# Performance work log

Hardware: AMD Instinct MI355X
Metric: run time of the kernel (lower is better)

Reference implementation:

```python
import jax, jax.numpy as jnp
import numpy as np

TEMPERATURE = 0.07
N, D = 16384, 128
NUM_CLASSES = 100


def setup_inputs() -> dict:
    key = jax.random.key(0)
    kf, kl = jax.random.split(key)
    features = jax.random.normal(kf, (N, D), dtype=jnp.float32)
    labels = jax.random.randint(kl, (N,), 0, NUM_CLASSES, dtype=jnp.int64)
    return {"features": features, "labels": labels}


def reference(features, labels):
    # L2-normalize along feature dim (torch F.normalize, eps=1e-12)
    norm = jnp.linalg.norm(features, axis=1, keepdims=True)
    feats = features / jnp.maximum(norm, 1e-12)
    # [N, N] cosine similarity scaled by temperature
    sim = jnp.matmul(feats, feats.T) / TEMPERATURE
    # positive mask: same label, diagonal zeroed
    lab = labels.reshape(-1, 1)
    mask = (lab == lab.T).astype(sim.dtype)
    n = sim.shape[0]
    mask = mask * (1.0 - jnp.eye(n, dtype=sim.dtype))
    exp_sim = jnp.exp(sim)
    # denominator uses (1 - mask): all non-positive pairs INCLUDING the diagonal
    denom = jnp.sum(exp_sim * (1.0 - mask), axis=1)
    numer = jnp.sum(exp_sim * mask, axis=1)
    loss = -jnp.log(numer / denom + 1e-08)
    return jnp.mean(loss)
```

## Files before the change

### kernel.cpp

```cpp
#include <hip/hip_runtime.h>
#include <hip/hip_bf16.h>
#include <cstdint>
#include <cstddef>


#define N_ROWS 16384
#define DIM    128
#define TILE   128
#define NTILES (N_ROWS / TILE)

#define FEAT_SCALE 4.5398164f

typedef __attribute__((ext_vector_type(8))) short bf16x8;
typedef __attribute__((ext_vector_type(4))) float f32x4;

typedef const __attribute__((address_space(1))) unsigned int* gas_ptr;
typedef __attribute__((address_space(3))) unsigned int* las_ptr;

__global__ __launch_bounds__(256) void k_normalize(const float* __restrict__ F,
                                                   __hip_bfloat16* __restrict__ G) {
    int tid  = threadIdx.x;
    int lane = tid & 63;
    int wave = tid >> 6;
    int row  = blockIdx.x * 4 + wave;
    const float2* src = (const float2*)(F + (size_t)row * DIM) + lane;
    float2 x = *src;
    float s = x.x * x.x + x.y * x.y;
#pragma unroll
    for (int i = 1; i < 64; i <<= 1) s += __shfl_xor(s, i, 64);
    float scale = FEAT_SCALE / fmaxf(sqrtf(s), 1e-12f);
    __hip_bfloat162 h;
    h.x = __float2bfloat16(x.x * scale);
    h.y = __float2bfloat16(x.y * scale);
    ((__hip_bfloat162*)(G + (size_t)row * DIM))[lane] = h;
}

template<bool ATOM>
__global__ __launch_bounds__(256, 2) void k_tiles(const __hip_bfloat16* __restrict__ G,
                                                  const int* __restrict__ lab,
                                                  float* __restrict__ pNum,
                                                  float* __restrict__ pTot) {
    int J = blockIdx.x, I = blockIdx.y;
    if (J < I) return;
    bool diag = (I == J);

    __shared__ __align__(16) char lds[65536 + 4096];
    char* ldsA = lds;
    char* ldsB = diag ? lds : (lds + 32768);
    float* sR = (float*)(lds + 65536);
    float* sC = (float*)(lds + 65536 + 2048);

    int tid = threadIdx.x;

    {
        const char* gA = (const char*)G + (size_t)I * TILE * DIM * 2;
#pragma unroll
        for (int p = 0; p < 8; ++p) {
            int o = p * 4096 + tid * 16;
            int so = o ^ (((o >> 8) & 7) << 4);
            __builtin_amdgcn_global_load_lds((gas_ptr)(gA + so), (las_ptr)(ldsA + o), 16, 0, 0);
        }
        if (!diag) {
            const char* gB = (const char*)G + (size_t)J * TILE * DIM * 2;
#pragma unroll
            for (int p = 0; p < 8; ++p) {
                int o = p * 4096 + tid * 16;
                int so = o ^ (((o >> 8) & 7) << 4);
                __builtin_amdgcn_global_load_lds((gas_ptr)(gB + so), (las_ptr)(ldsB + o), 16, 0, 0);
            }
        }
    }
    __syncthreads();

    int lane = tid & 63, w = tid >> 6;
    int wr = w >> 1, wc = w & 1;
    int lr = lane & 15, lhi = lane >> 4;

    f32x4 acc[4][4];
#pragma unroll
    for (int m = 0; m < 4; ++m)
#pragma unroll
        for (int n = 0; n < 4; ++n) acc[m][n] = (f32x4){0.f, 0.f, 0.f, 0.f};

#pragma unroll
    for (int kk = 0; kk < 4; ++kk) {
        bf16x8 a[4], b[4];
#pragma unroll
        for (int m = 0; m < 4; ++m) {
            int row = wr * 64 + m * 16 + lr;
            int lin = row * 256 + kk * 64 + lhi * 16;
            a[m] = *(const bf16x8*)(ldsA + (lin ^ ((row & 7) << 4)));
        }
#pragma unroll
        for (int n = 0; n < 4; ++n) {
            int row = wc * 64 + n * 16 + lr;
            int lin = row * 256 + kk * 64 + lhi * 16;
            b[n] = *(const bf16x8*)(ldsB + (lin ^ ((row & 7) << 4)));
        }
#pragma unroll
        for (int m = 0; m < 4; ++m)
#pragma unroll
            for (int n = 0; n < 4; ++n)
                acc[m][n] = __builtin_amdgcn_mfma_f32_16x16x32_bf16(a[m], b[n], acc[m][n], 0, 0, 0);
    }

    int rowbase = I * TILE + wr * 64;
    int colbase = J * TILE + wc * 64;

    int labr[4][4];
#pragma unroll
    for (int m = 0; m < 4; ++m)
#pragma unroll
        for (int r = 0; r < 4; ++r) labr[m][r] = lab[rowbase + m * 16 + lhi * 4 + r];

    float rn[4][4], rt[4][4], cn[4], ct[4];
#pragma unroll
    for (int m = 0; m < 4; ++m)
#pragma unroll
        for (int r = 0; r < 4; ++r) { rn[m][r] = 0.f; rt[m][r] = 0.f; }
#pragma unroll
    for (int n = 0; n < 4; ++n) { cn[n] = 0.f; ct[n] = 0.f; }

#pragma unroll
    for (int n = 0; n < 4; ++n) {
        int col = colbase + n * 16 + lr;
        int labc = lab[col];
#pragma unroll
        for (int m = 0; m < 4; ++m) {
            int row0 = rowbase + m * 16 + lhi * 4;
#pragma unroll
            for (int r = 0; r < 4; ++r) {
                float e = __builtin_amdgcn_exp2f(acc[m][n][r]);
                float te = ((row0 + r) != col) ? e : 0.f;
                float me = (labr[m][r] == labc) ? te : 0.f;
                rn[m][r] += me;  rt[m][r] += te;
                cn[n]    += me;  ct[n]    += te;
            }
        }
    }

#pragma unroll
    for (int m = 0; m < 4; ++m)
#pragma unroll
        for (int r = 0; r < 4; ++r) {
            float v1 = rn[m][r], v2 = rt[m][r];
#pragma unroll
            for (int s = 1; s < 16; s <<= 1) {
                v1 += __shfl_xor(v1, s, 64);
                v2 += __shfl_xor(v2, s, 64);
            }
            if (lr == 0) {
                int rowt = wr * 64 + m * 16 + lhi * 4 + r;
                sR[wc * 128 + rowt]       = v1;
                sR[256 + wc * 128 + rowt] = v2;
            }
        }
#pragma unroll
    for (int n = 0; n < 4; ++n) {
        float v1 = cn[n], v2 = ct[n];
        v1 += __shfl_xor(v1, 16, 64); v1 += __shfl_xor(v1, 32, 64);
        v2 += __shfl_xor(v2, 16, 64); v2 += __shfl_xor(v2, 32, 64);
        if (lhi == 0) {
            int colt = wc * 64 + n * 16 + lr;
            sC[wr * 128 + colt]       = v1;
            sC[256 + wr * 128 + colt] = v2;
        }
    }
    __syncthreads();

    if (tid < 128) {
        float num = sR[tid] + sR[128 + tid];
        float tot = sR[256 + tid] + sR[384 + tid];
        int row = I * TILE + tid;
        if (ATOM) { atomicAdd(&pNum[row], num); atomicAdd(&pTot[row], tot); }
        else {
            pNum[(size_t)J * N_ROWS + row] = num;
            pTot[(size_t)J * N_ROWS + row] = tot;
        }
    } else if (!diag) {
        int c = tid - 128;
        float num = sC[c] + sC[128 + c];
        float tot = sC[256 + c] + sC[384 + c];
        int col = J * TILE + c;
        if (ATOM) { atomicAdd(&pNum[col], num); atomicAdd(&pTot[col], tot); }
        else {
            pNum[(size_t)I * N_ROWS + col] = num;
            pTot[(size_t)I * N_ROWS + col] = tot;
        }
    }
}

template<bool ATOM>
__global__ __launch_bounds__(256) void k_rowloss(const float* __restrict__ pNum,
                                                 const float* __restrict__ pTot,
                                                 float* __restrict__ losses) {
    int row = blockIdx.x * 256 + threadIdx.x;
    float num = 0.f, tot = 0.f;
    if (ATOM) {
        num = pNum[row]; tot = pTot[row];
    } else {
        for (int k = 0; k < NTILES; ++k) {
            num += pNum[(size_t)k * N_ROWS + row];
            tot += pTot[(size_t)k * N_ROWS + row];
        }
    }
    float ediag = expf(14.285714285714286f);
    float denom = tot - num + ediag;
    losses[row] = -logf(num / denom + 1e-8f);
}

__global__ __launch_bounds__(1024) void k_mean(const float* __restrict__ losses,
                                               float* __restrict__ out) {
    int tid = threadIdx.x;
    float s = 0.f;
    for (int i = tid; i < N_ROWS; i += 1024) s += losses[i];
#pragma unroll
    for (int i = 1; i < 64; i <<= 1) s += __shfl_xor(s, i, 64);
    __shared__ float red[16];
    if ((tid & 63) == 0) red[tid >> 6] = s;
    __syncthreads();
    if (tid < 16) {
        float v = red[tid];
#pragma unroll
        for (int i = 1; i < 16; i <<= 1) v += __shfl_xor(v, i, 64);
        if (tid == 0) out[0] = v / (float)N_ROWS;
    }
}

extern "C" void kernel_launch(void* const* d_in, const int* in_sizes, int n_in,
                              void* d_out, int out_size, void* d_ws, size_t ws_size,
                              hipStream_t stream) {
    const float* F  = (const float*)d_in[0];
    const int* lab  = (const int*)d_in[1];
    float* out      = (float*)d_out;
    char* ws        = (char*)d_ws;

    __hip_bfloat16* G = (__hip_bfloat16*)ws;
    float* losses = (float*)(ws + (4 << 20));
    size_t offP = (4 << 20) + (64 << 10);

    k_normalize<<<N_ROWS / 4, 256, 0, stream>>>(F, G);

    bool partial = ws_size >= offP + ((size_t)16 << 20) + 1024;
    if (partial) {
        float* pNum = (float*)(ws + offP);
        float* pTot = (float*)(ws + offP + ((size_t)8 << 20));
        k_tiles<false><<<dim3(NTILES, NTILES), 256, 0, stream>>>(G, lab, pNum, pTot);
        k_rowloss<false><<<N_ROWS / 256, 256, 0, stream>>>(pNum, pTot, losses);
    } else {
        float* rN = (float*)(ws + offP);
        float* rT = (float*)(ws + offP + (64 << 10));
        hipMemsetAsync(rN, 0, 128 << 10, stream);
        k_tiles<true><<<dim3(NTILES, NTILES), 256, 0, stream>>>(G, lab, rN, rT);
        k_rowloss<true><<<N_ROWS / 256, 256, 0, stream>>>(rN, rT, losses);
    }
    k_mean<<<1, 1024, 0, stream>>>(losses, out);
}
```

Baseline: 223.0 us.

## Persist row tiles over column strips with double-buffered B loads and atomics

Replaces the 128x128 grid of upper-triangular tile blocks, half of which exit immediately, with a compact grid of 2112 blocks. Each block keeps one row tile's A fragments in registers and loops over up to four column tiles, prefetching the next B tile into a second LDS buffer while computing the current one. The non-diagonal exp path drops the diagonal check, and the per-tile partial-sum buffers are replaced by global atomics, which also merges the mean reduction into the row-loss kernel. This removes the empty blocks and repeated A loads, but adds per-tile block syncs, atomic traffic and fewer tiles of parallel work per block.

```diff
diff --git a/kernel.cpp b/kernel.cpp
--- a/kernel.cpp
+++ b/kernel.cpp
@@ -35,108 +35,167 @@
     ((__hip_bfloat162*)(G + (size_t)row * DIM))[lane] = h;
 }
 
-template<bool ATOM>
 __global__ __launch_bounds__(256, 2) void k_tiles(const __hip_bfloat16* __restrict__ G,
                                                   const int* __restrict__ lab,
-                                                  float* __restrict__ pNum,
-                                                  float* __restrict__ pTot) {
-    int J = blockIdx.x, I = blockIdx.y;
-    if (J < I) return;
-    bool diag = (I == J);
-
-    __shared__ __align__(16) char lds[65536 + 4096];
-    char* ldsA = lds;
-    char* ldsB = diag ? lds : (lds + 32768);
-    float* sR = (float*)(lds + 65536);
-    float* sC = (float*)(lds + 65536 + 2048);
+                                                  float* __restrict__ rN,
+                                                  float* __restrict__ rT) {
+    __shared__ __align__(16) char lds[65536 + 2048];
+    float* sRed = (float*)(lds + 65536);
 
     int tid = threadIdx.x;
 
+    int bid = blockIdx.x;
+    int u = bid >> 2, i2 = bid & 3;
+    int c = (int)((sqrtf(8.f * (float)u + 1.f) - 1.f) * 0.5f);
+    while ((c + 1) * (c + 2) / 2 <= u) ++c;
+    while (c * (c + 1) / 2 > u) --c;
+    int g = u - c * (c + 1) / 2;
+    int I = g * 4 + i2;
+    int J0 = (I > c * 4) ? I : c * 4;
+    int nj = c * 4 + 4 - J0;
+
+    const char* gbase = (const char*)G;
     {
-        const char* gA = (const char*)G + (size_t)I * TILE * DIM * 2;
+        const char* gA = gbase + (size_t)I * (TILE * DIM * 2);
+        const char* gB = gbase + (size_t)J0 * (TILE * DIM * 2);
 #pragma unroll
         for (int p = 0; p < 8; ++p) {
             int o = p * 4096 + tid * 16;
             int so = o ^ (((o >> 8) & 7) << 4);
-            __builtin_amdgcn_global_load_lds((gas_ptr)(gA + so), (las_ptr)(ldsA + o), 16, 0, 0);
-        }
-        if (!diag) {
-            const char* gB = (const char*)G + (size_t)J * TILE * DIM * 2;
+            __builtin_amdgcn_global_load_lds((gas_ptr)(gA + so), (las_ptr)(lds + o), 16, 0, 0);
+            __builtin_amdgcn_global_load_lds((gas_ptr)(gB + so), (las_ptr)(lds + 32768 + o), 16, 0, 0);
+        }
+    }
+
+    int lane = tid & 63, w = tid >> 6;
+    int wr = w >> 1, wc = w & 1;
+    int lr = lane & 15, lhi = lane >> 4;
+
+    __syncthreads();
+
+    bf16x8 afr[4][4];
+#pragma unroll
+    for (int m = 0; m < 4; ++m) {
+        int row = wr * 64 + m * 16 + lr;
+#pragma unroll
+        for (int kk = 0; kk < 4; ++kk) {
+            int lin = row * 256 + kk * 64 + lhi * 16;
+            afr[m][kk] = *(const bf16x8*)(lds + (lin ^ ((row & 7) << 4)));
+        }
+    }
+    int rowbase = I * TILE + wr * 64;
+    int labr[4][4];
+#pragma unroll
+    for (int m = 0; m < 4; ++m)
+#pragma unroll
+        for (int r = 0; r < 4; ++r) labr[m][r] = lab[rowbase + m * 16 + lhi * 4 + r];
+
+    float rn[4][4], rt[4][4];
+#pragma unroll
+    for (int m = 0; m < 4; ++m)
+#pragma unroll
+        for (int r = 0; r < 4; ++r) { rn[m][r] = 0.f; rt[m][r] = 0.f; }
+
+    __syncthreads();
+
+    for (int t = 0; t < nj; ++t) {
+        char* buf = lds + (((t & 1) ^ 1) << 15);
+        int Jt = J0 + t;
+
+        if (t + 1 < nj) {
+            const char* gB = gbase + (size_t)(Jt + 1) * (TILE * DIM * 2);
+            char* nbuf = lds + ((t & 1) << 15);
 #pragma unroll
             for (int p = 0; p < 8; ++p) {
                 int o = p * 4096 + tid * 16;
                 int so = o ^ (((o >> 8) & 7) << 4);
-                __builtin_amdgcn_global_load_lds((gas_ptr)(gB + so), (las_ptr)(ldsB + o), 16, 0, 0);
-            }
-        }
-    }
-    __syncthreads();
-
-    int lane = tid & 63, w = tid >> 6;
-    int wr = w >> 1, wc = w & 1;
-    int lr = lane & 15, lhi = lane >> 4;
-
-    f32x4 acc[4][4];
-#pragma unroll
-    for (int m = 0; m < 4; ++m)
-#pragma unroll
-        for (int n = 0; n < 4; ++n) acc[m][n] = (f32x4){0.f, 0.f, 0.f, 0.f};
-
-#pragma unroll
-    for (int kk = 0; kk < 4; ++kk) {
-        bf16x8 a[4], b[4];
-#pragma unroll
-        for (int m = 0; m < 4; ++m) {
-            int row = wr * 64 + m * 16 + lr;
-            int lin = row * 256 + kk * 64 + lhi * 16;
-            a[m] = *(const bf16x8*)(ldsA + (lin ^ ((row & 7) << 4)));
-        }
+                __builtin_amdgcn_global_load_lds((gas_ptr)(gB + so), (las_ptr)(nbuf + o), 16, 0, 0);
+            }
+        }
+        __builtin_amdgcn_sched_barrier(0);
+
+        int colbase = Jt * TILE + wc * 64;
+        int labc[4];
+#pragma unroll
+        for (int n = 0; n < 4; ++n) labc[n] = lab[colbase + n * 16 + lr];
+
+        f32x4 acc[4][4];
+#pragma unroll
+        for (int m = 0; m < 4; ++m)
+#pragma unroll
+            for (int n = 0; n < 4; ++n) acc[m][n] = (f32x4){0.f, 0.f, 0.f, 0.f};
+
+#pragma unroll
+        for (int kk = 0; kk < 4; ++kk) {
+            bf16x8 b[4];
+#pragma unroll
+            for (int n = 0; n < 4; ++n) {
+                int row = wc * 64 + n * 16 + lr;
+                int lin = row * 256 + kk * 64 + lhi * 16;
+                b[n] = *(const bf16x8*)(buf + (lin ^ ((row & 7) << 4)));
+            }
+#pragma unroll
+            for (int m = 0; m < 4; ++m)
+#pragma unroll
+                for (int n = 0; n < 4; ++n)
+                    acc[m][n] = __builtin_amdgcn_mfma_f32_16x16x32_bf16(afr[m][kk], b[n], acc[m][n], 0, 0, 0);
+        }
+
+        float cn[4] = {0.f, 0.f, 0.f, 0.f}, ct[4] = {0.f, 0.f, 0.f, 0.f};
+        bool isdiag = (Jt == I);
+        if (isdiag) {
+#pragma unroll
+            for (int n = 0; n < 4; ++n) {
+                int col = colbase + n * 16 + lr;
+#pragma unroll
+                for (int m = 0; m < 4; ++m) {
+                    int row0 = rowbase + m * 16 + lhi * 4;
+#pragma unroll
+                    for (int r = 0; r < 4; ++r) {
+                        float e = __builtin_amdgcn_exp2f(acc[m][n][r]);
+                        float te = ((row0 + r) != col) ? e : 0.f;
+                        float me = (labr[m][r] == labc[n]) ? te : 0.f;
+                        rn[m][r] += me;  rt[m][r] += te;
+                        cn[n]    += me;  ct[n]    += te;
+                    }
+                }
+            }
+        } else {
+#pragma unroll
+            for (int n = 0; n < 4; ++n) {
+#pragma unroll
+                for (int m = 0; m < 4; ++m) {
+#pragma unroll
+                    for (int r = 0; r < 4; ++r) {
+                        float e = __builtin_amdgcn_exp2f(acc[m][n][r]);
+                        float me = (labr[m][r] == labc[n]) ? e : 0.f;
+                        rn[m][r] += me;  rt[m][r] += e;
+                        cn[n]    += me;  ct[n]    += e;
+                    }
+                }
+            }
+        }
+
 #pragma unroll
         for (int n = 0; n < 4; ++n) {
-            int row = wc * 64 + n * 16 + lr;
-            int lin = row * 256 + kk * 64 + lhi * 16;
-            b[n] = *(const bf16x8*)(ldsB + (lin ^ ((row & 7) << 4)));
-        }
-#pragma unroll
-        for (int m = 0; m < 4; ++m)
-#pragma unroll
-            for (int n = 0; n < 4; ++n)
-                acc[m][n] = __builtin_amdgcn_mfma_f32_16x16x32_bf16(a[m], b[n], acc[m][n], 0, 0, 0);
-    }
-
-    int rowbase = I * TILE + wr * 64;
-    int colbase = J * TILE + wc * 64;
-
-    int labr[4][4];
-#pragma unroll
-    for (int m = 0; m < 4; ++m)
-#pragma unroll
-        for (int r = 0; r < 4; ++r) labr[m][r] = lab[rowbase + m * 16 + lhi * 4 + r];
-
-    float rn[4][4], rt[4][4], cn[4], ct[4];
-#pragma unroll
-    for (int m = 0; m < 4; ++m)
-#pragma unroll
-        for (int r = 0; r < 4; ++r) { rn[m][r] = 0.f; rt[m][r] = 0.f; }
-#pragma unroll
-    for (int n = 0; n < 4; ++n) { cn[n] = 0.f; ct[n] = 0.f; }
-
-#pragma unroll
-    for (int n = 0; n < 4; ++n) {
-        int col = colbase + n * 16 + lr;
-        int labc = lab[col];
-#pragma unroll
-        for (int m = 0; m < 4; ++m) {
-            int row0 = rowbase + m * 16 + lhi * 4;
-#pragma unroll
-            for (int r = 0; r < 4; ++r) {
-                float e = __builtin_amdgcn_exp2f(acc[m][n][r]);
-                float te = ((row0 + r) != col) ? e : 0.f;
-                float me = (labr[m][r] == labc) ? te : 0.f;
-                rn[m][r] += me;  rt[m][r] += te;
-                cn[n]    += me;  ct[n]    += te;
-            }
-        }
+            float v1 = cn[n], v2 = ct[n];
+            v1 += __shfl_xor(v1, 16, 64); v1 += __shfl_xor(v1, 32, 64);
+            v2 += __shfl_xor(v2, 16, 64); v2 += __shfl_xor(v2, 32, 64);
+            if (lhi == 0) {
+                int colt = wc * 64 + n * 16 + lr;
+                sRed[wr * 128 + colt]       = v1;
+                sRed[256 + wr * 128 + colt] = v2;
+            }
+        }
+        __syncthreads();
+        if (!isdiag && tid < 128) {
+            float num = sRed[tid] + sRed[128 + tid];
+            float tot = sRed[256 + tid] + sRed[384 + tid];
+            int col = Jt * TILE + tid;
+            atomicAdd(&rN[col], num);
+            atomicAdd(&rT[col], tot);
+        }
+        __syncthreads();
     }
 
 #pragma unroll
@@ -151,80 +210,39 @@
             }
             if (lr == 0) {
                 int rowt = wr * 64 + m * 16 + lhi * 4 + r;
-                sR[wc * 128 + rowt]       = v1;
-                sR[256 + wc * 128 + rowt] = v2;
-            }
-        }
-#pragma unroll
-    for (int n = 0; n < 4; ++n) {
-        float v1 = cn[n], v2 = ct[n];
-        v1 += __shfl_xor(v1, 16, 64); v1 += __shfl_xor(v1, 32, 64);
-        v2 += __shfl_xor(v2, 16, 64); v2 += __shfl_xor(v2, 32, 64);
-        if (lhi == 0) {
-            int colt = wc * 64 + n * 16 + lr;
-            sC[wr * 128 + colt]       = v1;
-            sC[256 + wr * 128 + colt] = v2;
-        }
-    }
-    __syncthreads();
-
+                sRed[wc * 128 + rowt]       = v1;
+                sRed[256 + wc * 128 + rowt] = v2;
+            }
+        }
+    __syncthreads();
     if (tid < 128) {
-        float num = sR[tid] + sR[128 + tid];
-        float tot = sR[256 + tid] + sR[384 + tid];
+        float num = sRed[tid] + sRed[128 + tid];
+        float tot = sRed[256 + tid] + sRed[384 + tid];
         int row = I * TILE + tid;
-        if (ATOM) { atomicAdd(&pNum[row], num); atomicAdd(&pTot[row], tot); }
-        else {
-            pNum[(size_t)J * N_ROWS + row] = num;
-            pTot[(size_t)J * N_ROWS + row] = tot;
-        }
-    } else if (!diag) {
-        int c = tid - 128;
-        float num = sC[c] + sC[128 + c];
-        float tot = sC[256 + c] + sC[384 + c];
-        int col = J * TILE + c;
-        if (ATOM) { atomicAdd(&pNum[col], num); atomicAdd(&pTot[col], tot); }
-        else {
-            pNum[(size_t)I * N_ROWS + col] = num;
-            pTot[(size_t)I * N_ROWS + col] = tot;
-        }
-    }
-}
-
-template<bool ATOM>
-__global__ __launch_bounds__(256) void k_rowloss(const float* __restrict__ pNum,
-                                                 const float* __restrict__ pTot,
-                                                 float* __restrict__ losses) {
+        atomicAdd(&rN[row], num);
+        atomicAdd(&rT[row], tot);
+    }
+}
+
+__global__ __launch_bounds__(256) void k_rowloss(const float* __restrict__ rN,
+                                                 const float* __restrict__ rT,
+                                                 float* __restrict__ accum) {
     int row = blockIdx.x * 256 + threadIdx.x;
-    float num = 0.f, tot = 0.f;
-    if (ATOM) {
-        num = pNum[row]; tot = pTot[row];
-    } else {
-        for (int k = 0; k < NTILES; ++k) {
-            num += pNum[(size_t)k * N_ROWS + row];
-            tot += pTot[(size_t)k * N_ROWS + row];
-        }
-    }
+    float num = rN[row], tot = rT[row];
     float ediag = expf(14.285714285714286f);
     float denom = tot - num + ediag;
-    losses[row] = -logf(num / denom + 1e-8f);
-}
-
-__global__ __launch_bounds__(1024) void k_mean(const float* __restrict__ losses,
-                                               float* __restrict__ out) {
-    int tid = threadIdx.x;
-    float s = 0.f;
-    for (int i = tid; i < N_ROWS; i += 1024) s += losses[i];
-#pragma unroll
-    for (int i = 1; i < 64; i <<= 1) s += __shfl_xor(s, i, 64);
-    __shared__ float red[16];
-    if ((tid & 63) == 0) red[tid >> 6] = s;
-    __syncthreads();
-    if (tid < 16) {
-        float v = red[tid];
-#pragma unroll
-        for (int i = 1; i < 16; i <<= 1) v += __shfl_xor(v, i, 64);
-        if (tid == 0) out[0] = v / (float)N_ROWS;
-    }
+    float loss = -logf(num / denom + 1e-8f);
+#pragma unroll
+    for (int i = 1; i < 64; i <<= 1) loss += __shfl_xor(loss, i, 64);
+    __shared__ float red[4];
+    if ((threadIdx.x & 63) == 0) red[threadIdx.x >> 6] = loss;
+    __syncthreads();
+    if (threadIdx.x == 0)
+        atomicAdd(accum, red[0] + red[1] + red[2] + red[3]);
+}
+
+__global__ void k_final(const float* __restrict__ accum, float* __restrict__ out) {
+    out[0] = accum[0] / (float)N_ROWS;
 }
 
 extern "C" void kernel_launch(void* const* d_in, const int* in_sizes, int n_in,
@@ -236,23 +254,16 @@
     char* ws        = (char*)d_ws;
 
     __hip_bfloat16* G = (__hip_bfloat16*)ws;
-    float* losses = (float*)(ws + (4 << 20));
-    size_t offP = (4 << 20) + (64 << 10);
+    float* rN    = (float*)(ws + (4 << 20));
+    float* rT    = rN + N_ROWS;
+    float* accum = rT + N_ROWS;
 
     k_normalize<<<N_ROWS / 4, 256, 0, stream>>>(F, G);
-
-    bool partial = ws_size >= offP + ((size_t)16 << 20) + 1024;
-    if (partial) {
-        float* pNum = (float*)(ws + offP);
-        float* pTot = (float*)(ws + offP + ((size_t)8 << 20));
-        k_tiles<false><<<dim3(NTILES, NTILES), 256, 0, stream>>>(G, lab, pNum, pTot);
-        k_rowloss<false><<<N_ROWS / 256, 256, 0, stream>>>(pNum, pTot, losses);
-    } else {
-        float* rN = (float*)(ws + offP);
-        float* rT = (float*)(ws + offP + (64 << 10));
-        hipMemsetAsync(rN, 0, 128 << 10, stream);
-        k_tiles<true><<<dim3(NTILES, NTILES), 256, 0, stream>>>(G, lab, rN, rT);
-        k_rowloss<true><<<N_ROWS / 256, 256, 0, stream>>>(rN, rT, losses);
-    }
-    k_mean<<<1, 1024, 0, stream>>>(losses, out);
-}
+    hipMemsetAsync(rN, 0, (size_t)N_ROWS * 2 * sizeof(float) + 16, stream);
+
+    int nblocks = 2112;
+    k_tiles<<<nblocks, 256, 0, stream>>>(G, lab, rN, rT);
+
+    k_rowloss<<<N_ROWS / 256, 256, 0, stream>>>(rN, rT, accum);
+    k_final<<<1, 1, 0, stream>>>(accum, out);
+}
```

Result: no change. 227.0 us (+1.8%).
